# Performance work log

Hardware: AMD Instinct MI355X
Metric: run time of the kernel (lower is better)

Reference implementation:

```python
import jax, jax.numpy as jnp
import numpy as np

N, E, G, D, L = 10000, 160000, 100, 128, 5
LMAX, SHD, VOCAB = 2, 9, 10
S3 = 3.0 ** 0.5


def _sph(v):
    # e3nn spherical harmonics, normalize=True, normalization='norm' (||Y_l||=1), lmax=2
    r = jnp.linalg.norm(v, axis=-1, keepdims=True)
    u = v / jnp.maximum(r, 1e-12)
    x, y, z = u[:, 0], u[:, 1], u[:, 2]
    y2 = jnp.stack([S3 * x * z, S3 * x * y, y * y - 0.5 * (x * x + z * z), S3 * y * z, 0.5 * S3 * (z * z - x * x)], axis=-1)
    return jnp.concatenate([jnp.ones_like(u[:, :1]), u, y2], axis=-1)  # [E,9]


def _sh_scale(s, w):
    # FullyConnectedTensorProduct(sh, 1x0e, sh): per-l scaling by weight w [.,3]
    return jnp.concatenate([s[:, 0:1] * w[:, 0:1], s[:, 1:4] * w[:, 1:2], s[:, 4:9] * w[:, 2:3]], axis=-1)


def _smean(src, idx, n):
    s = jax.ops.segment_sum(src, idx, num_segments=n)
    c = jax.ops.segment_sum(jnp.ones((src.shape[0], 1), src.dtype), idx, num_segments=n)
    return s / jnp.maximum(c, 1.0)


def _mlp(x, w1, b1, w2, b2, last_act=False):
    h = jax.nn.silu(x @ w1 + b1)
    o = h @ w2 + b2
    return jax.nn.silu(o) if last_act else o


def _forward(atoms, edge_index, batch_ids, pos, emb_table, Wsi1, bsi1, Wsi2, bsi2, WsiC1, bsiC1, WsiC2, bsiC2, Wm1, bm1, Wm2, bm2, Wp1, bp1, Wp2, bp2, Wn1, bn1, Wn2, bn2, Ws1, bs1, Ws2, bs2, Wpred, bpred):
    row, col = edge_index[0], edge_index[1]
    feat = emb_table[atoms]                                  # [N,D]
    # --- SH_INIT ---
    dpos = pos[row] - pos[col]
    dist = jnp.linalg.norm(dpos, axis=-1, keepdims=True)
    msg = _mlp(jnp.concatenate([dist, feat[row], feat[col]], axis=-1), Wsi1, bsi1, Wsi2, bsi2)
    dsh = _sh_scale(jax.lax.stop_gradient(_sph(dpos)), msg)
    sh = _smean(dsh, row, N)                                 # [N,9]
    pos_com = _smean(pos, batch_ids, G)[batch_ids]
    sh = sh + _sh_scale(jax.lax.stop_gradient(_sph(pos - pos_com)), _mlp(feat, WsiC1, bsiC1, WsiC2, bsiC2))
    sh = sh.at[:, :LMAX * LMAX].set(0.0)                     # all_ell=False: keep only highest l
    # --- stacked HEGNN layers via scan ---
    def body(carry, p):
        feat, pos, sh = carry
        wm1, cm1, wm2, cm2, wp1, cp1, wp2, cp2, wn1, cn1, wn2, cn2, ws1, cs1, ws2, cs2 = p
        dp = pos[row] - pos[col]
        d2 = jnp.sum(dp * dp, axis=-1, keepdims=True)        # squared distance
        t = sh[row] * sh[col]
        ip = jnp.concatenate([jnp.sum(t[:, 0:1], -1, keepdims=True), jnp.sum(t[:, 1:4], -1, keepdims=True), jnp.sum(t[:, 4:9], -1, keepdims=True)], axis=-1)
        m = _mlp(jnp.concatenate([feat[row], feat[col], d2, ip], axis=-1), wm1, cm1, wm2, cm2, last_act=True)
        dp = dp * _mlp(m, wp1, cp1, wp2, cp2)
        ds = _sh_scale(sh[row] - sh[col], _mlp(m, ws1, cs1, ws2, cs2))
        m_agg = _smean(m, row, N)
        p_agg = _smean(dp, row, N)
        s_agg = _smean(ds, row, N)
        sh = sh + s_agg
        pos = pos + p_agg
        feat = _mlp(jnp.concatenate([feat, m_agg], axis=-1), wn1, cn1, wn2, cn2)
        return (feat, pos, sh), None
    (feat, pos, sh), _ = jax.lax.scan(body, (feat, pos, sh), (Wm1, bm1, Wm2, bm2, Wp1, bp1, Wp2, bp2, Wn1, bn1, Wn2, bn2, Ws1, bs1, Ws2, bs2))
    # --- equivariant sum-pool + linear pred ---
    pooled = jax.ops.segment_sum(jnp.concatenate([feat, pos, sh], axis=-1), batch_ids, num_segments=G)
    return pooled @ Wpred + bpred                            # [G,1]


def setup_inputs():
    ks = iter(jax.random.split(jax.random.key(0), 48))
    def nrm(shape):
        return jax.random.normal(next(ks), shape, jnp.float32)
    def w(shape):
        return nrm(shape) / np.float32(np.sqrt(shape[-2]))
    z = lambda *s: jnp.zeros(s, jnp.float32)
    inp = dict(
        atoms=jax.random.randint(next(ks), (N,), 0, VOCAB),
        edge_index=jax.random.randint(next(ks), (2, E), 0, N),
        batch_ids=jnp.sort(jax.random.randint(next(ks), (N,), 0, G)),
        pos=nrm((N, 3)),
        emb_table=nrm((VOCAB, D)) * 0.1,
    )
    inp.update(Wsi1=w((2 * D + 1, D)), bsi1=z(D), Wsi2=w((D, LMAX + 1)), bsi2=z(LMAX + 1),
               WsiC1=w((D, D)), bsiC1=z(D), WsiC2=w((D, LMAX + 1)), bsiC2=z(LMAX + 1))
    inp.update(Wm1=w((L, 2 * D + 1 + LMAX + 1, D)), bm1=z(L, D), Wm2=w((L, D, D)), bm2=z(L, D),
               Wp1=w((L, D, D)), bp1=z(L, D), Wp2=w((L, D, 1)), bp2=z(L, 1),
               Wn1=w((L, 2 * D, D)), bn1=z(L, D), Wn2=w((L, D, D)), bn2=z(L, D),
               Ws1=w((L, D, D)), bs1=z(L, D), Ws2=w((L, D, LMAX + 1)), bs2=z(L, LMAX + 1),
               Wpred=w((D + 3 + SHD, 1)), bpred=z(1))
    return inp


def reference(atoms, edge_index, batch_ids, pos, emb_table, Wsi1, bsi1, Wsi2, bsi2, WsiC1, bsiC1, WsiC2, bsiC2, Wm1, bm1, Wm2, bm2, Wp1, bp1, Wp2, bp2, Wn1, bn1, Wn2, bn2, Ws1, bs1, Ws2, bs2, Wpred, bpred):
    return _forward(atoms, edge_index, batch_ids, pos, emb_table, Wsi1, bsi1, Wsi2, bsi2, WsiC1, bsiC1, WsiC2, bsiC2, Wm1, bm1, Wm2, bm2, Wp1, bp1, Wp2, bp2, Wn1, bn1, Wn2, bn2, Ws1, bs1, Ws2, bs2, Wpred, bpred)
```

## Files before the change

kernel.cpp:

```cpp
#include <hip/hip_runtime.h>
#include <math.h>

#define NA 10000
#define NE 160000
#define NG 100
#define DF 128
#define NL 5
#define NAP 10112
#define NSB 40

typedef __attribute__((ext_vector_type(8))) short bfx8;
typedef __attribute__((ext_vector_type(4))) float f32x4;

__device__ __forceinline__ float silu_f(float x) {
    return x / (1.0f + __expf(-x));
}

__device__ __forceinline__ unsigned short f2bf(float x) {
    unsigned u = __builtin_bit_cast(unsigned, x);
    u = (u + 0x7FFFu + ((u >> 16) & 1u)) >> 16;
    return (unsigned short)u;
}
__device__ __forceinline__ float bf2f(unsigned short h) {
    unsigned u = ((unsigned)h) << 16;
    return __builtin_bit_cast(float, u);
}
__device__ __forceinline__ unsigned packbf(float lo, float hi) {
    return (unsigned)f2bf(lo) | ((unsigned)f2bf(hi) << 16);
}

__device__ __forceinline__ void sph9(float dx, float dy, float dz, float* s) {
    float r = sqrtf(dx * dx + dy * dy + dz * dz);
    float inv = 1.0f / fmaxf(r, 1e-12f);
    float x = dx * inv, y = dy * inv, z = dz * inv;
    const float S3 = 1.7320508075688772f;
    s[0] = 1.0f;
    s[1] = x; s[2] = y; s[3] = z;
    s[4] = S3 * x * z;
    s[5] = S3 * x * y;
    s[6] = y * y - 0.5f * (x * x + z * z);
    s[7] = S3 * y * z;
    s[8] = 0.5f * S3 * (z * z - x * x);
}

#define OFF_SIRC  0
#define OFF_SICTR 32768
#define LBASE     49152
#define LOFF_MRC  0
#define LOFF_M2   32768
#define LOFF_P1   49152
#define LOFF_S1   65536
#define LOFF_N1   81920
#define LOFF_N2   114688
#define LSIZE     131072
#define WT_TOTAL  704512

__global__ void k_prep_w(const float* __restrict__ Wsi1, const float* __restrict__ WsiC1,
                         const float* __restrict__ Wm1, const float* __restrict__ Wm2,
                         const float* __restrict__ Wp1, const float* __restrict__ Ws1,
                         const float* __restrict__ Wn1, const float* __restrict__ Wn2,
                         unsigned short* __restrict__ WT) {
    int flat = blockIdx.x * 256 + threadIdx.x;
    if (flat >= WT_TOTAL) return;
    float v = 0.0f;
    if (flat < OFF_SICTR) {
        int half = flat >> 14;
        int o = flat & 16383;
        int n = o >> 7, k = o & 127;
        v = Wsi1[(k + 1 + half * 128) * 128 + n];
    } else if (flat < LBASE) {
        int o = flat - OFF_SICTR;
        int n = o >> 7, k = o & 127;
        v = WsiC1[k * 128 + n];
    } else {
        int t = flat - LBASE;
        int lyr = t / LSIZE;
        int o = t % LSIZE;
        if (o < LOFF_M2) {
            int half = o >> 14;
            int o2 = o & 16383;
            int n = o2 >> 7, k = o2 & 127;
            v = Wm1[(size_t)lyr * 33280 + (k + half * 128) * 128 + n];
        } else if (o < LOFF_P1) {
            int o2 = o - LOFF_M2; int n = o2 >> 7, k = o2 & 127;
            v = Wm2[(size_t)lyr * 16384 + k * 128 + n];
        } else if (o < LOFF_S1) {
            int o2 = o - LOFF_P1; int n = o2 >> 7, k = o2 & 127;
            v = Wp1[(size_t)lyr * 16384 + k * 128 + n];
        } else if (o < LOFF_N1) {
            int o2 = o - LOFF_S1; int n = o2 >> 7, k = o2 & 127;
            v = Ws1[(size_t)lyr * 16384 + k * 128 + n];
        } else if (o < LOFF_N2) {
            int o2 = o - LOFF_N1; int n = o2 >> 8, k = o2 & 255;
            v = Wn1[(size_t)lyr * 32768 + k * 128 + n];
        } else {
            int o2 = o - LOFF_N2; int n = o2 >> 7, k = o2 & 127;
            v = Wn2[(size_t)lyr * 16384 + k * 128 + n];
        }
    }
    WT[flat] = f2bf(v);
}

__global__ __launch_bounds__(256) void k_fgemm(
    const unsigned short* __restrict__ Ab,
    const unsigned short* __restrict__ WT2,
    unsigned short* __restrict__ F12)
{
    __shared__ unsigned short As[128 * 40];
    __shared__ unsigned short Bs[128 * 40];
    const unsigned short* WTp = WT2 + (size_t)blockIdx.y * 16384;
    unsigned short* Cb = F12 + (size_t)blockIdx.y * NAP * 128;

    const int tid = threadIdx.x;
    const int m0 = blockIdx.x * 128;
    const int mlo = tid >> 2;
    const int part = tid & 3;
    const int w = tid >> 6, l = tid & 63;
    const int quad = l >> 4, lm = l & 15;
    const int wm = (w >> 1) * 64, wn = (w & 1) * 64;

    f32x4 acc[4][4] = {};
#pragma unroll 1
    for (int c = 0; c < 4; c++) {
        const int k0 = c * 32;
#pragma unroll
        for (int i = 0; i < 2; i++) {
            const int m = mlo + i * 64;
            *(uint4*)&As[m * 40 + part * 8] =
                *(const uint4*)(Ab + (size_t)(m0 + m) * 128 + k0 + part * 8);
            *(uint4*)&Bs[m * 40 + part * 8] =
                *(const uint4*)(WTp + (size_t)m * 128 + k0 + part * 8);
        }
        __syncthreads();
        bfx8 a[4], b[4];
#pragma unroll
        for (int i = 0; i < 4; i++) a[i] = *(const bfx8*)&As[(wm + i * 16 + lm) * 40 + quad * 8];
#pragma unroll
        for (int j = 0; j < 4; j++) b[j] = *(const bfx8*)&Bs[(wn + j * 16 + lm) * 40 + quad * 8];
#pragma unroll
        for (int i = 0; i < 4; i++)
#pragma unroll
            for (int j = 0; j < 4; j++)
                acc[i][j] = __builtin_amdgcn_mfma_f32_16x16x32_bf16(a[i], b[j], acc[i][j], 0, 0, 0);
        __syncthreads();
    }
#pragma unroll
    for (int i = 0; i < 4; i++) {
        const int rbase = wm + i * 16 + quad * 4;
#pragma unroll
        for (int r = 0; r < 4; r++) {
            const int e = m0 + rbase + r;
#pragma unroll
            for (int j = 0; j < 4; j++)
                Cb[(size_t)e * 128 + wn + j * 16 + lm] = f2bf(acc[i][j][r]);
        }
    }
}

template <int KP, bool ACT, int NOUT, bool F32OUT>
__global__ __launch_bounds__(256) void gemm_mfma(
    const unsigned short* __restrict__ Ab,
    const unsigned short* __restrict__ WT,
    const float* __restrict__ bias, int M,
    unsigned short* __restrict__ Cb, float* __restrict__ Cf,
    const float* __restrict__ W2, const float* __restrict__ b2,
    float* __restrict__ outS)
{
    constexpr int NO = (NOUT > 0) ? NOUT : 1;
    __shared__ unsigned short As[128 * 40];
    __shared__ unsigned short Bs[128 * 40];
    __shared__ float W2s[NOUT > 0 ? 128 * NO : 1];
    __shared__ float red[NOUT > 0 ? 128 * 8 * NO : 1];

    const int tid = threadIdx.x;
    const int m0 = blockIdx.x * 128;
    const int mlo = tid >> 2;
    const int part = tid & 3;

    if (NOUT > 0) {
        for (int t = tid; t < 128 * NO; t += 256) W2s[t] = W2[t];
    }

    const int w = tid >> 6, l = tid & 63;
    const int quad = l >> 4, lm = l & 15;
    const int wm = (w >> 1) * 64, wn = (w & 1) * 64;

    float bv[4];
#pragma unroll
    for (int j = 0; j < 4; j++) bv[j] = bias[wn + j * 16 + lm];

    f32x4 acc[4][4] = {};
    constexpr int NCH = KP / 32;
#pragma unroll 1
    for (int c = 0; c < NCH; c++) {
        const int k0 = c * 32;
#pragma unroll
        for (int i = 0; i < 2; i++) {
            const int m = mlo + i * 64;
            *(uint4*)&As[m * 40 + part * 8] =
                *(const uint4*)(Ab + (size_t)(m0 + m) * KP + k0 + part * 8);
            *(uint4*)&Bs[m * 40 + part * 8] =
                *(const uint4*)(WT + (size_t)m * KP + k0 + part * 8);
        }
        __syncthreads();
        bfx8 a[4], b[4];
#pragma unroll
        for (int i = 0; i < 4; i++) a[i] = *(const bfx8*)&As[(wm + i * 16 + lm) * 40 + quad * 8];
#pragma unroll
        for (int j = 0; j < 4; j++) b[j] = *(const bfx8*)&Bs[(wn + j * 16 + lm) * 40 + quad * 8];
#pragma unroll
        for (int i = 0; i < 4; i++)
#pragma unroll
            for (int j = 0; j < 4; j++)
                acc[i][j] = __builtin_amdgcn_mfma_f32_16x16x32_bf16(a[i], b[j], acc[i][j], 0, 0, 0);
        __syncthreads();
    }

    if (NOUT > 0) {
        const int slot = (w & 1) * 4 + (lm >> 2);
#pragma unroll
        for (int i = 0; i < 4; i++) {
#pragma unroll
            for (int r = 0; r < 4; r++) {
                const int rowL = wm + i * 16 + quad * 4 + r;
                float ps[NO];
#pragma unroll
                for (int o = 0; o < NO; o++) ps[o] = 0.0f;
#pragma unroll
                for (int j = 0; j < 4; j++) {
                    float v = silu_f(acc[i][j][r] + bv[j]);
                    const int colg = wn + j * 16 + lm;
#pragma unroll
                    for (int o = 0; o < NO; o++) ps[o] += v * W2s[colg * NO + o];
                }
#pragma unroll
                for (int off = 1; off <= 2; off <<= 1)
#pragma unroll
                    for (int o = 0; o < NO; o++) ps[o] += __shfl_xor(ps[o], off, 64);
                if ((lm & 3) == 0)
#pragma unroll
                    for (int o = 0; o < NO; o++)
                        red[(rowL * 8 + slot) * NO + o] = ps[o];
            }
        }
        __syncthreads();
        for (int t = tid; t < 128 * NO; t += 256) {
            int rowL = t / NO, o = t - rowL * NO;
            float s = 0.0f;
#pragma unroll
            for (int k = 0; k < 8; k++) s += red[(rowL * 8 + k) * NO + o];
            int e = m0 + rowL;
            if (e < M) outS[(size_t)e * NO + o] = s + b2[o];
        }
    } else {
#pragma unroll
        for (int i = 0; i < 4; i++) {
            const int rbase = wm + i * 16 + quad * 4;
#pragma unroll
            for (int r = 0; r < 4; r++) {
                const int e = m0 + rbase + r;
                if (e >= M) continue;
#pragma unroll
                for (int j = 0; j < 4; j++) {
                    float v = acc[i][j][r] + bv[j];
                    if (ACT) v = silu_f(v);
                    const int colg = wn + j * 16 + lm;
                    Cb[(size_t)e * 128 + colg] = f2bf(v);
                    if (F32OUT) Cf[(size_t)e * 128 + colg] = v;
                }
            }
        }
    }
}

__global__ __launch_bounds__(256) void k_edge_h(
    const int* __restrict__ rowI, const int* __restrict__ colI,
    const unsigned short* __restrict__ F12,
    const float* __restrict__ pos, const float* __restrict__ sh,
    const float* __restrict__ wtail,
    const float* __restrict__ b1,
    unsigned short* __restrict__ bufHb)
{
    __shared__ float Wt[4][128];
    __shared__ float B1[128];
    int tid = threadIdx.x;
    if (tid < 128) B1[tid] = b1[tid];
    for (int t = tid; t < 512; t += 256) Wt[t >> 7][t & 127] = wtail[t];
    __syncthreads();

    int eloc = tid >> 1;
    int half = tid & 1;
    int e = blockIdx.x * 128 + eloc;
    int r = rowI[e], c = colI[e];

    float dx = pos[r * 3 + 0] - pos[c * 3 + 0];
    float dy = pos[r * 3 + 1] - pos[c * 3 + 1];
    float dz = pos[r * 3 + 2] - pos[c * 3 + 2];
    float d2 = dx * dx + dy * dy + dz * dz;
    const float* sr = sh + (size_t)r * 9;
    const float* sc = sh + (size_t)c * 9;
    float ip0 = sr[0] * sc[0];
    float ip1 = sr[1] * sc[1] + sr[2] * sc[2] + sr[3] * sc[3];
    float ip2 = sr[4] * sc[4] + sr[5] * sc[5] + sr[6] * sc[6] + sr[7] * sc[7] + sr[8] * sc[8];

    const unsigned short* f1 = F12 + (size_t)r * 128 + half * 64;
    const unsigned short* f2 = F12 + (size_t)NAP * 128 + (size_t)c * 128 + half * 64;
    unsigned short* outp = bufHb + (size_t)e * 128 + half * 64;
    const int jb = half * 64;

#pragma unroll
    for (int blk = 0; blk < 8; blk++) {
        uint4 a = *(const uint4*)(f1 + blk * 8);
        uint4 b = *(const uint4*)(f2 + blk * 8);
        unsigned av[4] = {a.x, a.y, a.z, a.w};
        unsigned bvv[4] = {b.x, b.y, b.z, b.w};
        unsigned ov[4];
#pragma unroll
        for (int q = 0; q < 4; q++) {
            int j0 = jb + blk * 8 + q * 2;
            float h0 = bf2f((unsigned short)(av[q] & 0xFFFFu)) + bf2f((unsigned short)(bvv[q] & 0xFFFFu))
                     + d2 * Wt[0][j0] + ip0 * Wt[1][j0] + ip1 * Wt[2][j0] + ip2 * Wt[3][j0] + B1[j0];
            float h1 = bf2f((unsigned short)(av[q] >> 16)) + bf2f((unsigned short)(bvv[q] >> 16))
                     + d2 * Wt[0][j0 + 1] + ip0 * Wt[1][j0 + 1] + ip1 * Wt[2][j0 + 1] + ip2 * Wt[3][j0 + 1] + B1[j0 + 1];
            ov[q] = packbf(silu_f(h0), silu_f(h1));
        }
        *(uint4*)(outp + blk * 8) = make_uint4(ov[0], ov[1], ov[2], ov[3]);
    }
}

__global__ __launch_bounds__(256) void k_edge_si(
    const int* __restrict__ rowI, const int* __restrict__ colI,
    const unsigned short* __restrict__ F12,
    const float* __restrict__ pos,
    const float* __restrict__ Wsi1,
    const float* __restrict__ b1,
    const float* __restrict__ W2,
    const float* __restrict__ b2,
    float* __restrict__ outS)
{
    __shared__ float Wd[128];
    __shared__ float B1[128];
    __shared__ float W2s[128 * 3];
    int tid = threadIdx.x;
    if (tid < 128) { Wd[tid] = Wsi1[tid]; B1[tid] = b1[tid]; }
    for (int t = tid; t < 384; t += 256) W2s[t] = W2[t];
    __syncthreads();

    int eloc = tid >> 1;
    int half = tid & 1;
    int e = blockIdx.x * 128 + eloc;
    int r = rowI[e], c = colI[e];

    float dx = pos[r * 3 + 0] - pos[c * 3 + 0];
    float dy = pos[r * 3 + 1] - pos[c * 3 + 1];
    float dz = pos[r * 3 + 2] - pos[c * 3 + 2];
    float dist = sqrtf(dx * dx + dy * dy + dz * dz);

    const unsigned short* f1 = F12 + (size_t)r * 128 + half * 64;
    const unsigned short* f2 = F12 + (size_t)NAP * 128 + (size_t)c * 128 + half * 64;
    const int jb = half * 64;

    float ps[3] = {0.0f, 0.0f, 0.0f};
#pragma unroll
    for (int blk = 0; blk < 8; blk++) {
        uint4 a = *(const uint4*)(f1 + blk * 8);
        uint4 b = *(const uint4*)(f2 + blk * 8);
        unsigned av[4] = {a.x, a.y, a.z, a.w};
        unsigned bvv[4] = {b.x, b.y, b.z, b.w};
#pragma unroll
        for (int q = 0; q < 4; q++) {
            int j0 = jb + blk * 8 + q * 2;
            float h0 = silu_f(bf2f((unsigned short)(av[q] & 0xFFFFu)) + bf2f((unsigned short)(bvv[q] & 0xFFFFu))
                              + dist * Wd[j0] + B1[j0]);
            float h1 = silu_f(bf2f((unsigned short)(av[q] >> 16)) + bf2f((unsigned short)(bvv[q] >> 16))
                              + dist * Wd[j0 + 1] + B1[j0 + 1]);
#pragma unroll
            for (int o = 0; o < 3; o++)
                ps[o] += h0 * W2s[j0 * 3 + o] + h1 * W2s[(j0 + 1) * 3 + o];
        }
    }
#pragma unroll
    for (int o = 0; o < 3; o++) ps[o] += __shfl_xor(ps[o], 1, 64);
    if (half == 0) {
#pragma unroll
        for (int o = 0; o < 3; o++) outS[(size_t)e * 3 + o] = ps[o] + b2[o];
    }
}

__global__ void k_count_edges(const int* __restrict__ row, int* __restrict__ cnt) {
    int e = blockIdx.x * blockDim.x + threadIdx.x;
    if (e < NE) atomicAdd(&cnt[row[e]], 1);
}

__global__ void k_scan_block(const int* __restrict__ cnt, int* __restrict__ ptr,
                             int* __restrict__ btot) {
    __shared__ int s[256];
    int tid = threadIdx.x;
    int i = blockIdx.x * 256 + tid;
    int v = (i < NA) ? cnt[i] : 0;
    s[tid] = v;
    __syncthreads();
    for (int off = 1; off < 256; off <<= 1) {
        int t = (tid >= off) ? s[tid - off] : 0;
        __syncthreads();
        s[tid] += t;
        __syncthreads();
    }
    if (i < NA) ptr[i] = s[tid] - v;
    if (tid == 255) btot[blockIdx.x] = s[255];
}

__global__ void k_scan_tot(int* __restrict__ btot) {
    int lane = threadIdx.x;
    int v = (lane < NSB) ? btot[lane] : 0;
    int orig = v;
    for (int off = 1; off < 64; off <<= 1) {
        int t = __shfl_up(v, off, 64);
        if (lane >= off) v += t;
    }
    if (lane < NSB) btot[lane] = v - orig;
}

__global__ void k_scan_add(int* __restrict__ ptr, const int* __restrict__ btot) {
    int i = blockIdx.x * 256 + threadIdx.x;
    if (i < NA) ptr[i] += btot[i >> 8];
    if (i == 0) ptr[NA] = NE;
}

__global__ void k_copy_cursor(const int* __restrict__ ptr, int* __restrict__ cursor) {
    int i = blockIdx.x * 256 + threadIdx.x;
    if (i < NA) cursor[i] = ptr[i];
}

__global__ void k_sort(const int* __restrict__ row, const int* __restrict__ col,
                       int* __restrict__ cursor,
                       int* __restrict__ row_s, int* __restrict__ col_s) {
    int e = blockIdx.x * blockDim.x + threadIdx.x;
    if (e >= NE) return;
    int r = row[e];
    int p = atomicAdd(&cursor[r], 1);
    row_s[p] = r;
    col_s[p] = col[e];
}

__global__ void k_gptr(const int* __restrict__ bid, int* __restrict__ gptr) {
    int n = blockIdx.x * blockDim.x + threadIdx.x;
    if (n >= NA) return;
    int b = bid[n];
    int bp = (n == 0) ? -1 : bid[n - 1];
    for (int g = bp + 1; g <= b; g++) gptr[g] = n;
    if (n == NA - 1)
        for (int g = b + 1; g <= NG; g++) gptr[g] = NA;
}

__global__ void k_init_feat(const int* __restrict__ atoms,
                            const float* __restrict__ emb,
                            float* __restrict__ feat, unsigned short* __restrict__ featb) {
    int idx = blockIdx.x * blockDim.x + threadIdx.x;
    if (idx >= NA * DF) return;
    float v = emb[atoms[idx >> 7] * DF + (idx & 127)];
    feat[idx] = v;
    featb[idx] = f2bf(v);
}

__global__ void k_copy_pos(const float* __restrict__ pos, float* __restrict__ posc) {
    int idx = blockIdx.x * blockDim.x + threadIdx.x;
    if (idx < NA * 3) posc[idx] = pos[idx];
}

__global__ void k_com_g(const float* __restrict__ pos, const int* __restrict__ gptr,
                        float* __restrict__ com) {
    int g = blockIdx.x;
    int lane = threadIdx.x;
    int s0 = gptr[g], s1 = gptr[g + 1];
    float sx = 0.0f, sy = 0.0f, sz = 0.0f;
    for (int n = s0 + lane; n < s1; n += 64) {
        sx += pos[n * 3 + 0];
        sy += pos[n * 3 + 1];
        sz += pos[n * 3 + 2];
    }
#pragma unroll
    for (int off = 32; off > 0; off >>= 1) {
        sx += __shfl_down(sx, off, 64);
        sy += __shfl_down(sy, off, 64);
        sz += __shfl_down(sz, off, 64);
    }
    if (lane == 0) {
        float cinv = 1.0f / fmaxf((float)(s1 - s0), 1.0f);
        com[g * 3 + 0] = sx * cinv;
        com[g * 3 + 1] = sy * cinv;
        com[g * 3 + 2] = sz * cinv;
    }
}

__global__ void k_gather_sph(const int* __restrict__ ptr, const int* __restrict__ col_s,
                             const float* __restrict__ pos, const float* __restrict__ msg,
                             float* __restrict__ sh_mean) {
    int n = blockIdx.x;
    int lane = threadIdx.x;
    int s0 = ptr[n], s1 = ptr[n + 1];
    float px = pos[n * 3 + 0], py = pos[n * 3 + 1], pz = pos[n * 3 + 2];
    float a[9];
#pragma unroll
    for (int j = 0; j < 9; j++) a[j] = 0.0f;
    for (int e = s0 + lane; e < s1; e += 64) {
        int c = col_s[e];
        float dx = px - pos[c * 3 + 0];
        float dy = py - pos[c * 3 + 1];
        float dz = pz - pos[c * 3 + 2];
        float s[9];
        sph9(dx, dy, dz, s);
        float w0 = msg[e * 3 + 0], w1 = msg[e * 3 + 1], w2 = msg[e * 3 + 2];
        a[0] += s[0] * w0;
        a[1] += s[1] * w1; a[2] += s[2] * w1; a[3] += s[3] * w1;
        a[4] += s[4] * w2; a[5] += s[5] * w2; a[6] += s[6] * w2;
        a[7] += s[7] * w2; a[8] += s[8] * w2;
    }
#pragma unroll
    for (int off = 32; off > 0; off >>= 1)
#pragma unroll
        for (int j = 0; j < 9; j++) a[j] += __shfl_down(a[j], off, 64);
    if (lane == 0) {
        float cinv = 1.0f / fmaxf((float)(s1 - s0), 1.0f);
#pragma unroll
        for (int j = 0; j < 9; j++) sh_mean[(size_t)n * 9 + j] = a[j] * cinv;
    }
}

__global__ void k_sh_finish(const float* __restrict__ sh_mean,
                            const float* __restrict__ pos, const float* __restrict__ com,
                            const int* __restrict__ bid, const float* __restrict__ msgC,
                            float* __restrict__ sh) {
    int n = blockIdx.x * blockDim.x + threadIdx.x;
    if (n >= NA) return;
    int b = bid[n];
    float dx = pos[n * 3 + 0] - com[b * 3 + 0];
    float dy = pos[n * 3 + 1] - com[b * 3 + 1];
    float dz = pos[n * 3 + 2] - com[b * 3 + 2];
    float s[9];
    sph9(dx, dy, dz, s);
    float w2 = msgC[n * 3 + 2];
    sh[n * 9 + 0] = 0.0f;
    sh[n * 9 + 1] = 0.0f;
    sh[n * 9 + 2] = 0.0f;
    sh[n * 9 + 3] = 0.0f;
#pragma unroll
    for (int j = 4; j < 9; j++)
        sh[n * 9 + j] = sh_mean[(size_t)n * 9 + j] + s[j] * w2;
}

__global__ __launch_bounds__(128) void k_gather_nx(
    const int* __restrict__ ptr, const int* __restrict__ col_s,
    const unsigned short* __restrict__ bufMb, const unsigned short* __restrict__ featb,
    const float* __restrict__ pos, const float* __restrict__ sh,
    const float* __restrict__ psc, const float* __restrict__ ssc,
    unsigned short* __restrict__ Xnb,
    float* __restrict__ pos_new, float* __restrict__ sh_new)
{
    int n = blockIdx.x;
    int tid = threadIdx.x;
    int s0 = ptr[n], s1 = ptr[n + 1];
    float cinv = 1.0f / fmaxf((float)(s1 - s0), 1.0f);

    float sum = 0.0f;
    for (int e = s0; e < s1; e++) sum += bf2f(bufMb[(size_t)e * 128 + tid]);
    Xnb[(size_t)n * 256 + tid] = featb[(size_t)n * 128 + tid];
    Xnb[(size_t)n * 256 + 128 + tid] = f2bf(sum * cinv);

    if (tid < 64) {
        int lane = tid;
        float px = pos[n * 3 + 0], py = pos[n * 3 + 1], pz = pos[n * 3 + 2];
        float shn[9];
#pragma unroll
        for (int j = 0; j < 9; j++) shn[j] = sh[(size_t)n * 9 + j];
        float a[12];
#pragma unroll
        for (int j = 0; j < 12; j++) a[j] = 0.0f;
        for (int e = s0 + lane; e < s1; e += 64) {
            int c = col_s[e];
            float p = psc[e];
            a[0] += (px - pos[c * 3 + 0]) * p;
            a[1] += (py - pos[c * 3 + 1]) * p;
            a[2] += (pz - pos[c * 3 + 2]) * p;
            float w0 = ssc[e * 3 + 0], w1 = ssc[e * 3 + 1], w2 = ssc[e * 3 + 2];
            const float* sc = sh + (size_t)c * 9;
            a[3]  += (shn[0] - sc[0]) * w0;
            a[4]  += (shn[1] - sc[1]) * w1;
            a[5]  += (shn[2] - sc[2]) * w1;
            a[6]  += (shn[3] - sc[3]) * w1;
            a[7]  += (shn[4] - sc[4]) * w2;
            a[8]  += (shn[5] - sc[5]) * w2;
            a[9]  += (shn[6] - sc[6]) * w2;
            a[10] += (shn[7] - sc[7]) * w2;
            a[11] += (shn[8] - sc[8]) * w2;
        }
#pragma unroll
        for (int off = 32; off > 0; off >>= 1)
#pragma unroll
            for (int j = 0; j < 12; j++) a[j] += __shfl_down(a[j], off, 64);
        if (lane == 0) {
            pos_new[n * 3 + 0] = px + a[0] * cinv;
            pos_new[n * 3 + 1] = py + a[1] * cinv;
            pos_new[n * 3 + 2] = pz + a[2] * cinv;
#pragma unroll
            for (int j = 0; j < 9; j++) sh_new[(size_t)n * 9 + j] = shn[j] + a[3 + j] * cinv;
        }
    }
}

__global__ __launch_bounds__(192) void k_pool_pred(
    const int* __restrict__ gptr, const float* __restrict__ feat,
    const float* __restrict__ pos, const float* __restrict__ sh,
    const float* __restrict__ Wp, const float* __restrict__ bp,
    float* __restrict__ out) {
    __shared__ float pl[140];
    int g = blockIdx.x;
    int c = threadIdx.x;
    int s0 = gptr[g], s1 = gptr[g + 1];
    if (c < 140) {
        float sum = 0.0f;
        for (int n = s0; n < s1; n++) {
            float v;
            if (c < 128)      v = feat[(size_t)n * 128 + c];
            else if (c < 131) v = pos[n * 3 + (c - 128)];
            else              v = sh[(size_t)n * 9 + (c - 131)];
            sum += v;
        }
        pl[c] = sum;
    }
    __syncthreads();
    if (c < 64) {
        float s = 0.0f;
        for (int k = c; k < 140; k += 64) s += pl[k] * Wp[k];
#pragma unroll
        for (int off = 32; off > 0; off >>= 1) s += __shfl_down(s, off, 64);
        if (c == 0) out[g] = s + bp[0];
    }
}

extern "C" void kernel_launch(void* const* d_in, const int* in_sizes, int n_in,
                              void* d_out, int out_size, void* d_ws, size_t ws_size,
                              hipStream_t stream) {
    const int*   atoms  = (const int*)d_in[0];
    const int*   eidx   = (const int*)d_in[1];
    const int*   row    = eidx;
    const int*   col    = eidx + NE;
    const int*   bid    = (const int*)d_in[2];
    const float* pos_in = (const float*)d_in[3];
    const float* emb    = (const float*)d_in[4];
    const float* Wsi1   = (const float*)d_in[5];
    const float* bsi1   = (const float*)d_in[6];
    const float* Wsi2   = (const float*)d_in[7];
    const float* bsi2   = (const float*)d_in[8];
    const float* WsiC1  = (const float*)d_in[9];
    const float* bsiC1  = (const float*)d_in[10];
    const float* WsiC2  = (const float*)d_in[11];
    const float* bsiC2  = (const float*)d_in[12];
    const float* Wm1    = (const float*)d_in[13];
    const float* bm1    = (const float*)d_in[14];
    const float* Wm2    = (const float*)d_in[15];
    const float* bm2    = (const float*)d_in[16];
    const float* Wp1    = (const float*)d_in[17];
    const float* bp1    = (const float*)d_in[18];
    const float* Wp2    = (const float*)d_in[19];
    const float* bp2    = (const float*)d_in[20];
    const float* Wn1    = (const float*)d_in[21];
    const float* bn1    = (const float*)d_in[22];
    const float* Wn2    = (const float*)d_in[23];
    const float* bn2    = (const float*)d_in[24];
    const float* Ws1    = (const float*)d_in[25];
    const float* bs1    = (const float*)d_in[26];
    const float* Ws2    = (const float*)d_in[27];
    const float* bs2    = (const float*)d_in[28];
    const float* Wpred  = (const float*)d_in[29];
    const float* bpred  = (const float*)d_in[30];

    float* base = (float*)d_ws;
    size_t off = 0;
    auto alloc = [&](size_t nfl) { float* r = base + off; off += nfl; return r; };
    unsigned short* bufHb = (unsigned short*)alloc((size_t)NE * DF / 2);
    unsigned short* bufMb = (unsigned short*)alloc((size_t)NE * DF / 2);
    unsigned short* featb = (unsigned short*)alloc((size_t)NAP * DF / 2);
    unsigned short* hnb   = (unsigned short*)alloc((size_t)NAP * DF / 2);
    unsigned short* Xnb   = (unsigned short*)alloc((size_t)NAP * 256 / 2);
    unsigned short* F12   = (unsigned short*)alloc((size_t)NAP * 256 / 2);
    unsigned short* WT    = (unsigned short*)alloc(WT_TOTAL / 2);
    float* feat    = alloc((size_t)NAP * DF);
    float* sc3     = alloc((size_t)NE * 3);
    float* psc     = alloc(NE);
    float* pos0    = alloc((size_t)NA * 3 + 4);
    float* pos1    = alloc((size_t)NA * 3 + 4);
    float* sh0     = alloc((size_t)NA * 9 + 4);
    float* sh1     = alloc((size_t)NA * 9 + 4);
    float* sh_mean = alloc((size_t)NA * 9 + 4);
    float* com     = alloc(NG * 3 + 4);
    float* msgC    = alloc((size_t)NA * 3 + 4);
    int* cnt_row   = (int*)alloc(NA);
    int* ptr       = (int*)alloc(NA + 4);
    int* cursor    = (int*)alloc(NA);
    int* gptr      = (int*)alloc(NG + 4);
    int* row_s     = (int*)alloc(NE);
    int* col_s     = (int*)alloc(NE);
    int* btot      = (int*)alloc(64);

    const dim3 B256(256);
    const int gE = NE / 128;
    const int gN = NAP / 128;
    const dim3 gF(gN, 2);

    hipMemsetAsync(cnt_row, 0, NA * sizeof(int), stream);
    k_prep_w<<<(WT_TOTAL + 255) / 256, B256, 0, stream>>>(Wsi1, WsiC1, Wm1, Wm2, Wp1, Ws1, Wn1, Wn2, WT);
    k_init_feat<<<(NA * DF + 255) / 256, B256, 0, stream>>>(atoms, emb, feat, featb);
    k_copy_pos<<<(NA * 3 + 255) / 256, B256, 0, stream>>>(pos_in, pos0);
    k_count_edges<<<(NE + 255) / 256, B256, 0, stream>>>(row, cnt_row);
    k_scan_block<<<NSB, B256, 0, stream>>>(cnt_row, ptr, btot);
    k_scan_tot<<<1, 64, 0, stream>>>(btot);
    k_scan_add<<<NSB, B256, 0, stream>>>(ptr, btot);
    k_copy_cursor<<<NSB, B256, 0, stream>>>(ptr, cursor);
    k_sort<<<(NE + 255) / 256, B256, 0, stream>>>(row, col, cursor, row_s, col_s);
    k_gptr<<<(NA + 255) / 256, B256, 0, stream>>>(bid, gptr);
    k_com_g<<<NG, 64, 0, stream>>>(pos_in, gptr, com);

    k_fgemm<<<gF, B256, 0, stream>>>(featb, WT + OFF_SIRC, F12);
    k_edge_si<<<gE, B256, 0, stream>>>(row_s, col_s, F12, pos0, Wsi1, bsi1, Wsi2, bsi2, sc3);
    k_gather_sph<<<NA, 64, 0, stream>>>(ptr, col_s, pos0, sc3, sh_mean);
    gemm_mfma<128, true, 3, false><<<gN, B256, 0, stream>>>(
        featb, WT + OFF_SICTR, bsiC1, NA, nullptr, nullptr, WsiC2, bsiC2, msgC);
    k_sh_finish<<<(NA + 255) / 256, B256, 0, stream>>>(sh_mean, pos0, com, bid, msgC, sh0);

    float* posA = pos0; float* posB = pos1;
    float* shA = sh0;   float* shB = sh1;

    for (int l = 0; l < NL; l++) {
        const unsigned short* wtL = WT + LBASE + (size_t)l * LSIZE;
        const float* cm1 = bm1 + l * 128;
        const float* wtail = Wm1 + (size_t)l * 33280 + 256 * 128;
        const float* cm2 = bm2 + l * 128;
        const float* cp1 = bp1 + l * 128;
        const float* wp2 = Wp2 + (size_t)l * 128;
        const float* cp2 = bp2 + l;
        const float* cn1 = bn1 + l * 128;
        const float* cn2 = bn2 + l * 128;
        const float* cs1 = bs1 + l * 128;
        const float* ws2 = Ws2 + (size_t)l * 128 * 3;
        const float* cs2 = bs2 + l * 3;

        k_fgemm<<<gF, B256, 0, stream>>>(featb, wtL + LOFF_MRC, F12);
        k_edge_h<<<gE, B256, 0, stream>>>(row_s, col_s, F12, posA, shA, wtail, cm1, bufHb);
        gemm_mfma<128, true, 0, false><<<gE, B256, 0, stream>>>(
            bufHb, wtL + LOFF_M2, cm2, NE, bufMb, nullptr, nullptr, nullptr, nullptr);
        gemm_mfma<128, true, 1, false><<<gE, B256, 0, stream>>>(
            bufMb, wtL + LOFF_P1, cp1, NE, nullptr, nullptr, wp2, cp2, psc);
        gemm_mfma<128, true, 3, false><<<gE, B256, 0, stream>>>(
            bufMb, wtL + LOFF_S1, cs1, NE, nullptr, nullptr, ws2, cs2, sc3);
        k_gather_nx<<<NA, 128, 0, stream>>>(ptr, col_s, bufMb, featb, posA, shA, psc, sc3,
                                            Xnb, posB, shB);
        gemm_mfma<256, true, 0, false><<<gN, B256, 0, stream>>>(
            Xnb, wtL + LOFF_N1, cn1, NA, hnb, nullptr, nullptr, nullptr, nullptr);
        gemm_mfma<128, false, 0, true><<<gN, B256, 0, stream>>>(
            hnb, wtL + LOFF_N2, cn2, NA, featb, feat, nullptr, nullptr, nullptr);

        float* tp = posA; posA = posB; posB = tp;
        float* ts = shA;  shA = shB;  shB = ts;
    }

    k_pool_pred<<<NG, 192, 0, stream>>>(gptr, feat, posA, shA, Wpred, bpred, (float*)d_out);
}
```

Before: 1.042 ms.

## Fuse edge hidden-layer computation into the message second-layer GEMM

The per-edge first MLP layer (gathered F12 sums plus distance and SH-inner-product tail terms, then SiLU) is now computed directly into the shared-memory A tile of the second message GEMM, instead of being written to a separate bufHb buffer and read back. This removes a full E x 128 bf16 write and read per layer, plus one kernel launch. In exchange, the gather and SiLU work sits inside the GEMM k-loop with extra synchronisation, and the tile uses a K step of 32 with no double buffering, which may lower MFMA utilisation.

```diff
diff --git a/kernel.cpp b/kernel.cpp
--- a/kernel.cpp
+++ b/kernel.cpp
@@ -273,58 +273,121 @@
     }
 }
 
-__global__ __launch_bounds__(256) void k_edge_h(
+__global__ __launch_bounds__(256) void k_m2f(
     const int* __restrict__ rowI, const int* __restrict__ colI,
     const unsigned short* __restrict__ F12,
     const float* __restrict__ pos, const float* __restrict__ sh,
     const float* __restrict__ wtail,
     const float* __restrict__ b1,
-    unsigned short* __restrict__ bufHb)
+    const unsigned short* __restrict__ w2,
+    const float* __restrict__ b2,
+    unsigned short* __restrict__ bufMb)
 {
-    __shared__ float Wt[4][128];
+    __shared__ unsigned short As[128 * 40];
+    __shared__ unsigned short Bs[128 * 40];
+    __shared__ float Wtj[128][4];
     __shared__ float B1[128];
-    int tid = threadIdx.x;
+    __shared__ float tail4[128][4];
+
+    const int tid = threadIdx.x;
+    const int m0 = blockIdx.x * 128;
     if (tid < 128) B1[tid] = b1[tid];
-    for (int t = tid; t < 512; t += 256) Wt[t >> 7][t & 127] = wtail[t];
+    for (int t = tid; t < 512; t += 256) Wtj[t & 127][t >> 7] = wtail[t];
+
+    const int mlo = tid >> 2;
+    const int part = tid & 3;
+    const int er0 = rowI[m0 + mlo],      ec0 = colI[m0 + mlo];
+    const int er1 = rowI[m0 + mlo + 64], ec1 = colI[m0 + mlo + 64];
+
+    if (part == 0) {
+#pragma unroll
+        for (int i = 0; i < 2; i++) {
+            int r = i ? er1 : er0, c = i ? ec1 : ec0;
+            int erow = mlo + i * 64;
+            float dx = pos[r * 3 + 0] - pos[c * 3 + 0];
+            float dy = pos[r * 3 + 1] - pos[c * 3 + 1];
+            float dz = pos[r * 3 + 2] - pos[c * 3 + 2];
+            const float* sr = sh + (size_t)r * 9;
+            const float* sc = sh + (size_t)c * 9;
+            tail4[erow][0] = dx * dx + dy * dy + dz * dz;
+            tail4[erow][1] = sr[0] * sc[0];
+            tail4[erow][2] = sr[1] * sc[1] + sr[2] * sc[2] + sr[3] * sc[3];
+            tail4[erow][3] = sr[4] * sc[4] + sr[5] * sc[5] + sr[6] * sc[6]
+                           + sr[7] * sc[7] + sr[8] * sc[8];
+        }
+    }
+
+    const int w = tid >> 6, l = tid & 63;
+    const int quad = l >> 4, lm = l & 15;
+    const int wm = (w >> 1) * 64, wn = (w & 1) * 64;
+
+    float bv[4];
+#pragma unroll
+    for (int j = 0; j < 4; j++) bv[j] = b2[wn + j * 16 + lm];
+
     __syncthreads();
 
-    int eloc = tid >> 1;
-    int half = tid & 1;
-    int e = blockIdx.x * 128 + eloc;
-    int r = rowI[e], c = colI[e];
-
-    float dx = pos[r * 3 + 0] - pos[c * 3 + 0];
-    float dy = pos[r * 3 + 1] - pos[c * 3 + 1];
-    float dz = pos[r * 3 + 2] - pos[c * 3 + 2];
-    float d2 = dx * dx + dy * dy + dz * dz;
-    const float* sr = sh + (size_t)r * 9;
-    const float* sc = sh + (size_t)c * 9;
-    float ip0 = sr[0] * sc[0];
-    float ip1 = sr[1] * sc[1] + sr[2] * sc[2] + sr[3] * sc[3];
-    float ip2 = sr[4] * sc[4] + sr[5] * sc[5] + sr[6] * sc[6] + sr[7] * sc[7] + sr[8] * sc[8];
-
-    const unsigned short* f1 = F12 + (size_t)r * 128 + half * 64;
-    const unsigned short* f2 = F12 + (size_t)NAP * 128 + (size_t)c * 128 + half * 64;
-    unsigned short* outp = bufHb + (size_t)e * 128 + half * 64;
-    const int jb = half * 64;
-
-#pragma unroll
-    for (int blk = 0; blk < 8; blk++) {
-        uint4 a = *(const uint4*)(f1 + blk * 8);
-        uint4 b = *(const uint4*)(f2 + blk * 8);
-        unsigned av[4] = {a.x, a.y, a.z, a.w};
-        unsigned bvv[4] = {b.x, b.y, b.z, b.w};
-        unsigned ov[4];
-#pragma unroll
-        for (int q = 0; q < 4; q++) {
-            int j0 = jb + blk * 8 + q * 2;
-            float h0 = bf2f((unsigned short)(av[q] & 0xFFFFu)) + bf2f((unsigned short)(bvv[q] & 0xFFFFu))
-                     + d2 * Wt[0][j0] + ip0 * Wt[1][j0] + ip1 * Wt[2][j0] + ip2 * Wt[3][j0] + B1[j0];
-            float h1 = bf2f((unsigned short)(av[q] >> 16)) + bf2f((unsigned short)(bvv[q] >> 16))
-                     + d2 * Wt[0][j0 + 1] + ip0 * Wt[1][j0 + 1] + ip1 * Wt[2][j0 + 1] + ip2 * Wt[3][j0 + 1] + B1[j0 + 1];
-            ov[q] = packbf(silu_f(h0), silu_f(h1));
-        }
-        *(uint4*)(outp + blk * 8) = make_uint4(ov[0], ov[1], ov[2], ov[3]);
+    float t4a[4], t4b[4];
+    *(float4*)t4a = *(const float4*)tail4[mlo];
+    *(float4*)t4b = *(const float4*)tail4[mlo + 64];
+
+    f32x4 acc[4][4] = {};
+#pragma unroll 1
+    for (int c = 0; c < 4; c++) {
+        const int k0 = c * 32;
+        const int j0b = k0 + part * 8;
+#pragma unroll
+        for (int i = 0; i < 2; i++) {
+            const int erow = mlo + i * 64;
+            const int er = i ? er1 : er0;
+            const int ec = i ? ec1 : ec0;
+            const float* tl = i ? t4b : t4a;
+            uint4 a = *(const uint4*)(F12 + (size_t)er * 128 + j0b);
+            uint4 b = *(const uint4*)(F12 + (size_t)NAP * 128 + (size_t)ec * 128 + j0b);
+            unsigned av[4] = {a.x, a.y, a.z, a.w};
+            unsigned bvv[4] = {b.x, b.y, b.z, b.w};
+            unsigned ov[4];
+#pragma unroll
+            for (int q = 0; q < 4; q++) {
+                int j0 = j0b + q * 2;
+                float4 wj0 = *(const float4*)Wtj[j0];
+                float4 wj1 = *(const float4*)Wtj[j0 + 1];
+                float h0 = bf2f((unsigned short)(av[q] & 0xFFFFu)) + bf2f((unsigned short)(bvv[q] & 0xFFFFu))
+                         + tl[0] * wj0.x + tl[1] * wj0.y + tl[2] * wj0.z + tl[3] * wj0.w + B1[j0];
+                float h1 = bf2f((unsigned short)(av[q] >> 16)) + bf2f((unsigned short)(bvv[q] >> 16))
+                         + tl[0] * wj1.x + tl[1] * wj1.y + tl[2] * wj1.z + tl[3] * wj1.w + B1[j0 + 1];
+                ov[q] = packbf(silu_f(h0), silu_f(h1));
+            }
+            *(uint4*)&As[erow * 40 + part * 8] = make_uint4(ov[0], ov[1], ov[2], ov[3]);
+            *(uint4*)&Bs[erow * 40 + part * 8] =
+                *(const uint4*)(w2 + (size_t)erow * 128 + k0 + part * 8);
+        }
+        __syncthreads();
+        bfx8 a[4], b[4];
+#pragma unroll
+        for (int i = 0; i < 4; i++) a[i] = *(const bfx8*)&As[(wm + i * 16 + lm) * 40 + quad * 8];
+#pragma unroll
+        for (int j = 0; j < 4; j++) b[j] = *(const bfx8*)&Bs[(wn + j * 16 + lm) * 40 + quad * 8];
+#pragma unroll
+        for (int i = 0; i < 4; i++)
+#pragma unroll
+            for (int j = 0; j < 4; j++)
+                acc[i][j] = __builtin_amdgcn_mfma_f32_16x16x32_bf16(a[i], b[j], acc[i][j], 0, 0, 0);
+        __syncthreads();
+    }
+
+#pragma unroll
+    for (int i = 0; i < 4; i++) {
+        const int rbase = wm + i * 16 + quad * 4;
+#pragma unroll
+        for (int r = 0; r < 4; r++) {
+            const int e = m0 + rbase + r;
+#pragma unroll
+            for (int j = 0; j < 4; j++) {
+                float v = silu_f(acc[i][j][r] + bv[j]);
+                bufMb[(size_t)e * 128 + wn + j * 16 + lm] = f2bf(v);
+            }
+        }
     }
 }
 
@@ -678,7 +741,6 @@
     float* base = (float*)d_ws;
     size_t off = 0;
     auto alloc = [&](size_t nfl) { float* r = base + off; off += nfl; return r; };
-    unsigned short* bufHb = (unsigned short*)alloc((size_t)NE * DF / 2);
     unsigned short* bufMb = (unsigned short*)alloc((size_t)NE * DF / 2);
     unsigned short* featb = (unsigned short*)alloc((size_t)NAP * DF / 2);
     unsigned short* hnb   = (unsigned short*)alloc((size_t)NAP * DF / 2);
@@ -746,9 +808,8 @@
         const float* cs2 = bs2 + l * 3;
 
         k_fgemm<<<gF, B256, 0, stream>>>(featb, wtL + LOFF_MRC, F12);
-        k_edge_h<<<gE, B256, 0, stream>>>(row_s, col_s, F12, posA, shA, wtail, cm1, bufHb);
-        gemm_mfma<128, true, 0, false><<<gE, B256, 0, stream>>>(
-            bufHb, wtL + LOFF_M2, cm2, NE, bufMb, nullptr, nullptr, nullptr, nullptr);
+        k_m2f<<<gE, B256, 0, stream>>>(
+            row_s, col_s, F12, posA, shA, wtail, cm1, wtL + LOFF_M2, cm2, bufMb);
         gemm_mfma<128, true, 1, false><<<gE, B256, 0, stream>>>(
             bufMb, wtL + LOFF_P1, cp1, NE, nullptr, nullptr, wp2, cp2, psc);
         gemm_mfma<128, true, 3, false><<<gE, B256, 0, stream>>>(
```

Measured after the change: 994.5 us. 1.05x faster.
